# Performance work log

Hardware: AMD Instinct MI355X
Metric: run time of the kernel (lower is better)

The kernel has to match this reference:

```python
import jax, jax.numpy as jnp
import numpy as np

N_NODES = 50000
N_EDGES = 800000
D = 128


def setup_inputs() -> dict:
    key = jax.random.key(0)
    k1, k2, k3, k4 = jax.random.split(key, 4)
    feat = jax.random.normal(k1, (N_NODES, D), dtype=jnp.float32)
    W = jax.random.normal(k2, (D, D), dtype=jnp.float32) * (1.0 / np.sqrt(D))
    b = jnp.zeros((D,), dtype=jnp.float32)
    eps = jnp.zeros((1,), dtype=jnp.float32)
    src = jax.random.randint(k3, (N_EDGES,), 0, N_NODES, dtype=jnp.int64 if jax.config.jax_enable_x64 else jnp.int32)
    dst = jax.random.randint(k4, (N_EDGES,), 0, N_NODES, dtype=jnp.int64 if jax.config.jax_enable_x64 else jnp.int32)
    return {"feat": feat, "W": W, "b": b, "eps": eps, "src": src, "dst": dst}


def reference(feat, W, b, eps, src, dst):
    # message passing: m_e = feat[src_e]; neigh_i = sum_{e: dst_e = i} m_e
    msgs = feat[src]  # [E, D] gather
    neigh = jax.ops.segment_sum(msgs, dst, num_segments=N_NODES)  # [N, D]
    # eps-weighted residual: (1 + eps) * h_dst + neigh
    rst = (1.0 + eps) * feat + neigh  # eps is [1], broadcasts
    # apply_func: Dense(D)
    out = jnp.einsum('nd,de->ne', rst, W) + b
    return out
```

## Files before the change

### kernel.cpp

```cpp
#include <hip/hip_runtime.h>

#define D 128
#define CAP 32
#define OCAP 4096
#define TILE 32

typedef __attribute__((ext_vector_type(8))) short bf16x8;
typedef __attribute__((ext_vector_type(4))) float f32x4;

static __device__ inline short f2bf(float f) {
  union { float f; unsigned u; } v; v.f = f;
  unsigned r = v.u + 0x7FFF + ((v.u >> 16) & 1);
  return (short)(r >> 16);
}
static __device__ inline float bf_lo(unsigned u) {
  union { unsigned u; float f; } v; v.u = u << 16; return v.f;
}
static __device__ inline float bf_hi(unsigned u) {
  union { unsigned u; float f; } v; v.u = u & 0xFFFF0000u; return v.f;
}

static __device__ inline void wfrag_build_one(const float* __restrict__ W,
                                              uint4* __restrict__ wfrag, int t) {
  int c = t >> 8, h = (t >> 6) & 3, l = t & 63;
  int col = c * 16 + (l & 15);
  int k0 = h * 32 + (l >> 4) * 8;
  unsigned u[4];
  #pragma unroll
  for (int p = 0; p < 4; ++p) {
    unsigned lo = (unsigned short)f2bf(W[(k0 + 2 * p) * D + col]);
    unsigned hi = (unsigned short)f2bf(W[(k0 + 2 * p + 1) * D + col]);
    u[p] = lo | (hi << 16);
  }
  wfrag[t] = make_uint4(u[0], u[1], u[2], u[3]);
}

static __device__ inline void edge_insert(
    int s, int d, int* __restrict__ cnt, int* __restrict__ ocount,
    unsigned* __restrict__ oflow, unsigned short* __restrict__ permfix) {
  int c = atomicAdd(&cnt[d], 1);
  if (c < CAP) {
    permfix[(size_t)d * CAP + c] = (unsigned short)s;
  } else {
    int o = atomicAdd(ocount, 1);
    if (o < OCAP) oflow[o] = ((unsigned)d << 16) | (unsigned)s;
  }
}

__global__ __launch_bounds__(256) void build_kernel(
    const int* __restrict__ src, const int* __restrict__ dst,
    int* __restrict__ cnt, int* __restrict__ ocount, unsigned* __restrict__ oflow,
    unsigned short* __restrict__ permfix,
    const float* __restrict__ W, uint4* __restrict__ wfrag,
    const float* __restrict__ feat, uint4* __restrict__ featbf,
    int E, int ND8) {
  int i = blockIdx.x * 256 + threadIdx.x;
  int e0 = i * 4;
  if (e0 + 4 <= E) {
    int4 s4 = *(const int4*)&src[e0];
    int4 d4 = *(const int4*)&dst[e0];
    edge_insert(s4.x, d4.x, cnt, ocount, oflow, permfix);
    edge_insert(s4.y, d4.y, cnt, ocount, oflow, permfix);
    edge_insert(s4.z, d4.z, cnt, ocount, oflow, permfix);
    edge_insert(s4.w, d4.w, cnt, ocount, oflow, permfix);
  } else if (e0 < E) {
    for (int e = e0; e < E; ++e)
      edge_insert(src[e], dst[e], cnt, ocount, oflow, permfix);
  }
  if (i < ND8) {
    float4 u = ((const float4*)feat)[2 * i];
    float4 v = ((const float4*)feat)[2 * i + 1];
    unsigned w0 = (unsigned short)f2bf(u.x) | ((unsigned)(unsigned short)f2bf(u.y) << 16);
    unsigned w1 = (unsigned short)f2bf(u.z) | ((unsigned)(unsigned short)f2bf(u.w) << 16);
    unsigned w2 = (unsigned short)f2bf(v.x) | ((unsigned)(unsigned short)f2bf(v.y) << 16);
    unsigned w3 = (unsigned short)f2bf(v.z) | ((unsigned)(unsigned short)f2bf(v.w) << 16);
    featbf[i] = make_uint4(w0, w1, w2, w3);
  }
  if (i < 2048) wfrag_build_one(W, wfrag, i);
}

__global__ __launch_bounds__(256, 8) void fused_gather_gemm(
    const uint2* __restrict__ featbf, const float* __restrict__ eps,
    const float* __restrict__ bias, const int* __restrict__ cnt,
    const int* __restrict__ ocount, const unsigned* __restrict__ oflow,
    const unsigned short* __restrict__ permfix,
    const uint4* __restrict__ wfrag, float* __restrict__ out, int N) {
  __shared__ float xs[TILE][132];
  __shared__ float sbias[128];
  int tid = threadIdx.x;
  int base = blockIdx.x * TILE;
  if (tid < 128) sbias[tid] = bias[tid];
  float scale = 1.0f + eps[0];

  int g = tid >> 5, lane = tid & 31;
  for (int it = 0; it < TILE / 8; ++it) {
    int lr = it * 8 + g;
    int grow = base + lr;
    float4 acc = make_float4(0.f, 0.f, 0.f, 0.f);
    if (grow < N) {
      uint2 a0 = featbf[(size_t)grow * 32 + lane];
      acc.x = scale * bf_lo(a0.x);
      acc.y = scale * bf_hi(a0.x);
      acc.z = scale * bf_lo(a0.y);
      acc.w = scale * bf_hi(a0.y);
      int deg = cnt[grow];
      deg = (deg < CAP) ? deg : CAP;
      const unsigned short* pf = permfix + (size_t)grow * CAP;
      int j = 0;
      for (; j + 8 <= deg; j += 8) {
        uint4 pv = *(const uint4*)&pf[j];
        int s0 = pv.x & 0xFFFF, s1 = pv.x >> 16;
        int s2 = pv.y & 0xFFFF, s3 = pv.y >> 16;
        int s4 = pv.z & 0xFFFF, s5 = pv.z >> 16;
        int s6 = pv.w & 0xFFFF, s7 = pv.w >> 16;
        uint2 r0 = featbf[(size_t)s0 * 32 + lane];
        uint2 r1 = featbf[(size_t)s1 * 32 + lane];
        uint2 r2 = featbf[(size_t)s2 * 32 + lane];
        uint2 r3 = featbf[(size_t)s3 * 32 + lane];
        uint2 r4 = featbf[(size_t)s4 * 32 + lane];
        uint2 r5 = featbf[(size_t)s5 * 32 + lane];
        uint2 r6 = featbf[(size_t)s6 * 32 + lane];
        uint2 r7 = featbf[(size_t)s7 * 32 + lane];
        acc.x += bf_lo(r0.x) + bf_lo(r1.x) + bf_lo(r2.x) + bf_lo(r3.x)
               + bf_lo(r4.x) + bf_lo(r5.x) + bf_lo(r6.x) + bf_lo(r7.x);
        acc.y += bf_hi(r0.x) + bf_hi(r1.x) + bf_hi(r2.x) + bf_hi(r3.x)
               + bf_hi(r4.x) + bf_hi(r5.x) + bf_hi(r6.x) + bf_hi(r7.x);
        acc.z += bf_lo(r0.y) + bf_lo(r1.y) + bf_lo(r2.y) + bf_lo(r3.y)
               + bf_lo(r4.y) + bf_lo(r5.y) + bf_lo(r6.y) + bf_lo(r7.y);
        acc.w += bf_hi(r0.y) + bf_hi(r1.y) + bf_hi(r2.y) + bf_hi(r3.y)
               + bf_hi(r4.y) + bf_hi(r5.y) + bf_hi(r6.y) + bf_hi(r7.y);
      }
      if (j + 4 <= deg) {
        uint2 pv = *(const uint2*)&pf[j];
        int s0 = pv.x & 0xFFFF, s1 = pv.x >> 16;
        int s2 = pv.y & 0xFFFF, s3 = pv.y >> 16;
        uint2 r0 = featbf[(size_t)s0 * 32 + lane];
        uint2 r1 = featbf[(size_t)s1 * 32 + lane];
        uint2 r2 = featbf[(size_t)s2 * 32 + lane];
        uint2 r3 = featbf[(size_t)s3 * 32 + lane];
        acc.x += bf_lo(r0.x) + bf_lo(r1.x) + bf_lo(r2.x) + bf_lo(r3.x);
        acc.y += bf_hi(r0.x) + bf_hi(r1.x) + bf_hi(r2.x) + bf_hi(r3.x);
        acc.z += bf_lo(r0.y) + bf_lo(r1.y) + bf_lo(r2.y) + bf_lo(r3.y);
        acc.w += bf_hi(r0.y) + bf_hi(r1.y) + bf_hi(r2.y) + bf_hi(r3.y);
        j += 4;
      }
      for (; j < deg; ++j) {
        uint2 a = featbf[(size_t)pf[j] * 32 + lane];
        acc.x += bf_lo(a.x); acc.y += bf_hi(a.x);
        acc.z += bf_lo(a.y); acc.w += bf_hi(a.y);
      }
    }
    *(float4*)&xs[lr][lane * 4] = acc;
  }
  __syncthreads();

  int novf = *ocount;
  novf = (novf < OCAP) ? novf : OCAP;
  if (novf > 0) {
    if (tid < 32) {
      for (int o = 0; o < novf; ++o) {
        unsigned e = oflow[o];
        int d = (int)(e >> 16);
        if ((d / TILE) == (int)blockIdx.x) {
          int s = (int)(e & 0xFFFF);
          uint2 a = featbf[(size_t)s * 32 + tid];
          int r = d % TILE;
          xs[r][tid * 4 + 0] += bf_lo(a.x);
          xs[r][tid * 4 + 1] += bf_hi(a.x);
          xs[r][tid * 4 + 2] += bf_lo(a.y);
          xs[r][tid * 4 + 3] += bf_hi(a.y);
        }
      }
    }
    __syncthreads();
  }

  int w = tid >> 6;
  int l = tid & 63;
  int rowg = l >> 4, rl = l & 15;
  int rs = (w & 1) * 16;
  int cb = (w >> 1) * 4;

  bf16x8 a[4];
  #pragma unroll
  for (int h = 0; h < 4; ++h) {
    const float* p = &xs[rs + rl][h * 32 + rowg * 8];
    float4 u = *(const float4*)p;
    float4 v = *(const float4*)(p + 4);
    bf16x8 t;
    t[0] = f2bf(u.x); t[1] = f2bf(u.y); t[2] = f2bf(u.z); t[3] = f2bf(u.w);
    t[4] = f2bf(v.x); t[5] = f2bf(v.y); t[6] = f2bf(v.z); t[7] = f2bf(v.w);
    a[h] = t;
  }

  const bf16x8* wf = (const bf16x8*)wfrag;
  #pragma unroll
  for (int cl = 0; cl < 4; ++cl) {
    int c = cb + cl;
    float bb = sbias[c * 16 + rl];
    f32x4 acc = {bb, bb, bb, bb};
    #pragma unroll
    for (int h = 0; h < 4; ++h) {
      bf16x8 b = wf[(c * 4 + h) * 64 + l];
      acc = __builtin_amdgcn_mfma_f32_16x16x32_bf16(a[h], b, acc, 0, 0, 0);
    }
    #pragma unroll
    for (int r = 0; r < 4; ++r) {
      int row = base + rs + rowg * 4 + r;
      if (row < N) out[(size_t)row * D + c * 16 + rl] = acc[r];
    }
  }
}

__global__ __launch_bounds__(256) void init_out_kernel(
    const float* __restrict__ feat, const float* __restrict__ eps,
    float* __restrict__ out, int n4) {
  int i = blockIdx.x * blockDim.x + threadIdx.x;
  if (i >= n4) return;
  float scale = 1.0f + eps[0];
  float4 v = ((const float4*)feat)[i];
  v.x *= scale; v.y *= scale; v.z *= scale; v.w *= scale;
  ((float4*)out)[i] = v;
}

__global__ __launch_bounds__(256) void scatter_add_kernel(
    const float* __restrict__ feat, const int* __restrict__ src,
    const int* __restrict__ dst, float* __restrict__ out, int E) {
  int gid = blockIdx.x * blockDim.x + threadIdx.x;
  int e = gid >> 5;
  int lane = gid & 31;
  if (e >= E) return;
  int s = src[e], d = dst[e];
  float4 v = ((const float4*)(feat + (size_t)s * D))[lane];
  float* o = out + (size_t)d * D + lane * 4;
  unsafeAtomicAdd(o + 0, v.x);
  unsafeAtomicAdd(o + 1, v.y);
  unsafeAtomicAdd(o + 2, v.z);
  unsafeAtomicAdd(o + 3, v.w);
}

#define ROWS 64
__global__ __launch_bounds__(256) void gemm_inplace_kernel(
    float* __restrict__ out, const float* __restrict__ Wm,
    const float* __restrict__ bias, int N) {
  __shared__ float Ws[D * D];
  __shared__ float xs[ROWS * D];
  int tid = threadIdx.x;
  int base = blockIdx.x * ROWS;
  #pragma unroll
  for (int it = 0; it < 16; ++it) {
    int idx = tid + 256 * it;
    ((float4*)Ws)[idx] = ((const float4*)Wm)[idx];
  }
  #pragma unroll
  for (int it = 0; it < 8; ++it) {
    int idx = tid + 256 * it;
    int row = idx >> 5, c4 = idx & 31;
    float4 v = make_float4(0.f, 0.f, 0.f, 0.f);
    if (base + row < N) v = ((const float4*)(out + (size_t)(base + row) * D))[c4];
    ((float4*)xs)[row * 32 + c4] = v;
  }
  __syncthreads();
  int tc = tid & 31, tr = tid >> 5;
  float acc[8][4];
  #pragma unroll
  for (int r = 0; r < 8; ++r)
    #pragma unroll
    for (int i = 0; i < 4; ++i) acc[r][i] = 0.f;
  for (int k0 = 0; k0 < D; k0 += 4) {
    float4 f[8];
    #pragma unroll
    for (int r = 0; r < 8; ++r) f[r] = *(const float4*)&xs[(tr * 8 + r) * D + k0];
    float w[4][4];
    #pragma unroll
    for (int u = 0; u < 4; ++u)
      #pragma unroll
      for (int i = 0; i < 4; ++i) w[u][i] = Ws[(k0 + u) * D + tc + 32 * i];
    #pragma unroll
    for (int r = 0; r < 8; ++r)
      #pragma unroll
      for (int i = 0; i < 4; ++i) {
        acc[r][i] += f[r].x * w[0][i];
        acc[r][i] += f[r].y * w[1][i];
        acc[r][i] += f[r].z * w[2][i];
        acc[r][i] += f[r].w * w[3][i];
      }
  }
  float bv[4];
  #pragma unroll
  for (int i = 0; i < 4; ++i) bv[i] = bias[tc + 32 * i];
  #pragma unroll
  for (int r = 0; r < 8; ++r) {
    int row = base + tr * 8 + r;
    if (row < N) {
      #pragma unroll
      for (int i = 0; i < 4; ++i)
        out[(size_t)row * D + tc + 32 * i] = acc[r][i] + bv[i];
    }
  }
}

extern "C" void kernel_launch(void* const* d_in, const int* in_sizes, int n_in,
                              void* d_out, int out_size, void* d_ws, size_t ws_size,
                              hipStream_t stream) {
  const float* feat = (const float*)d_in[0];
  const float* Wm   = (const float*)d_in[1];
  const float* bias = (const float*)d_in[2];
  const float* eps  = (const float*)d_in[3];
  const int*   src  = (const int*)d_in[4];
  const int*   dst  = (const int*)d_in[5];
  float* out = (float*)d_out;

  int N = in_sizes[0] / D;
  int E = in_sizes[4];
  int ND8 = (N * D) / 8;

  size_t cnt_b    = (size_t)N * 4;
  size_t ocount_b = 4;
  size_t oflow_b  = (size_t)OCAP * 4;
  size_t perm_b   = (size_t)N * CAP * 2;
  size_t wfrag_off = (cnt_b + ocount_b + oflow_b + perm_b + 15) & ~(size_t)15;
  size_t featbf_off = wfrag_off + 2048 * 16;
  size_t needed = featbf_off + (size_t)N * D * 2;

  if (ws_size >= needed) {
    int* cnt = (int*)d_ws;
    int* ocount = cnt + N;
    unsigned* oflow = (unsigned*)(ocount + 1);
    unsigned short* permfix = (unsigned short*)(oflow + OCAP);
    uint4* wfrag = (uint4*)((char*)d_ws + wfrag_off);
    uint4* featbf = (uint4*)((char*)d_ws + featbf_off);

    hipMemsetAsync(cnt, 0, cnt_b + ocount_b, stream);

    int gmax = max((E + 3) / 4, ND8);
    build_kernel<<<(gmax + 255) / 256, 256, 0, stream>>>(
        src, dst, cnt, ocount, oflow, permfix, Wm, wfrag, feat, featbf, E, ND8);

    fused_gather_gemm<<<(N + TILE - 1) / TILE, 256, 0, stream>>>(
        (const uint2*)featbf, eps, bias, cnt, ocount, oflow, permfix, wfrag, out, N);
  } else {
    int n4 = (N * D) / 4;
    init_out_kernel<<<(n4 + 255) / 256, 256, 0, stream>>>(feat, eps, out, n4);
    long long total_threads = (long long)E * 32;
    int sblocks = (int)((total_threads + 255) / 256);
    scatter_add_kernel<<<sblocks, 256, 0, stream>>>(feat, src, dst, out, E);
    int gblocks2 = (N + ROWS - 1) / ROWS;
    gemm_inplace_kernel<<<gblocks2, 256, 0, stream>>>(out, Wm, bias, N);
  }
}
```

Baseline: 111.6 us.

## Partition edge insertion by destination across XCD-mapped block groups

Build kernel now launches 8 block groups, each scanning all edges but inserting only those whose destination bucket maps to its group, so atomics and adjacency writes for a destination stay within one XCD's L2. Feature conversion becomes a grid-stride loop. This trades 8x redundant reads of the dst array for better locality of atomic counters and permfix writes.

```diff
diff --git a/kernel.cpp b/kernel.cpp
--- a/kernel.cpp
+++ b/kernel.cpp
@@ -4,6 +4,7 @@
 #define CAP 32
 #define OCAP 4096
 #define TILE 32
+#define BPG 512
 
 typedef __attribute__((ext_vector_type(8))) short bf16x8;
 typedef __attribute__((ext_vector_type(4))) float f32x4;
@@ -33,18 +34,6 @@
     u[p] = lo | (hi << 16);
   }
   wfrag[t] = make_uint4(u[0], u[1], u[2], u[3]);
-}
-
-static __device__ inline void edge_insert(
-    int s, int d, int* __restrict__ cnt, int* __restrict__ ocount,
-    unsigned* __restrict__ oflow, unsigned short* __restrict__ permfix) {
-  int c = atomicAdd(&cnt[d], 1);
-  if (c < CAP) {
-    permfix[(size_t)d * CAP + c] = (unsigned short)s;
-  } else {
-    int o = atomicAdd(ocount, 1);
-    if (o < OCAP) oflow[o] = ((unsigned)d << 16) | (unsigned)s;
-  }
 }
 
 __global__ __launch_bounds__(256) void build_kernel(
@@ -54,27 +43,32 @@
     const float* __restrict__ W, uint4* __restrict__ wfrag,
     const float* __restrict__ feat, uint4* __restrict__ featbf,
     int E, int ND8) {
+  int grp = blockIdx.x & 7;
+  int tidg = (blockIdx.x >> 3) * 256 + threadIdx.x;
+  int nthg = BPG * 256;
+  for (int e = tidg; e < E; e += nthg) {
+    int d = dst[e];
+    if (((d >> 5) & 7) == grp) {
+      int s = src[e];
+      int c = atomicAdd(&cnt[d], 1);
+      if (c < CAP) {
+        permfix[(size_t)d * CAP + c] = (unsigned short)s;
+      } else {
+        int o = atomicAdd(ocount, 1);
+        if (o < OCAP) oflow[o] = ((unsigned)d << 16) | (unsigned)s;
+      }
+    }
+  }
   int i = blockIdx.x * 256 + threadIdx.x;
-  int e0 = i * 4;
-  if (e0 + 4 <= E) {
-    int4 s4 = *(const int4*)&src[e0];
-    int4 d4 = *(const int4*)&dst[e0];
-    edge_insert(s4.x, d4.x, cnt, ocount, oflow, permfix);
-    edge_insert(s4.y, d4.y, cnt, ocount, oflow, permfix);
-    edge_insert(s4.z, d4.z, cnt, ocount, oflow, permfix);
-    edge_insert(s4.w, d4.w, cnt, ocount, oflow, permfix);
-  } else if (e0 < E) {
-    for (int e = e0; e < E; ++e)
-      edge_insert(src[e], dst[e], cnt, ocount, oflow, permfix);
-  }
-  if (i < ND8) {
-    float4 u = ((const float4*)feat)[2 * i];
-    float4 v = ((const float4*)feat)[2 * i + 1];
+  int nth = gridDim.x * 256;
+  for (int t = i; t < ND8; t += nth) {
+    float4 u = ((const float4*)feat)[2 * t];
+    float4 v = ((const float4*)feat)[2 * t + 1];
     unsigned w0 = (unsigned short)f2bf(u.x) | ((unsigned)(unsigned short)f2bf(u.y) << 16);
     unsigned w1 = (unsigned short)f2bf(u.z) | ((unsigned)(unsigned short)f2bf(u.w) << 16);
     unsigned w2 = (unsigned short)f2bf(v.x) | ((unsigned)(unsigned short)f2bf(v.y) << 16);
     unsigned w3 = (unsigned short)f2bf(v.z) | ((unsigned)(unsigned short)f2bf(v.w) << 16);
-    featbf[i] = make_uint4(w0, w1, w2, w3);
+    featbf[t] = make_uint4(w0, w1, w2, w3);
   }
   if (i < 2048) wfrag_build_one(W, wfrag, i);
 }
@@ -333,8 +327,7 @@
 
     hipMemsetAsync(cnt, 0, cnt_b + ocount_b, stream);
 
-    int gmax = max((E + 3) / 4, ND8);
-    build_kernel<<<(gmax + 255) / 256, 256, 0, stream>>>(
+    build_kernel<<<8 * BPG, 256, 0, stream>>>(
         src, dst, cnt, ocount, oflow, permfix, Wm, wfrag, feat, featbf, E, ND8);
 
     fused_gather_gemm<<<(N + TILE - 1) / TILE, 256, 0, stream>>>(
```

Result: faster. 92.72 us (-16.9%).
